# Kernel optimization log

Measured on AMD Instinct MI355X. Metric: run time of the kernel, lower is better.

Reference implementation:

```python
import jax, jax.numpy as jnp
import numpy as np

NEAR_THRESHOLD = 0.3
NUM_HEADING_BIN = 12
NUM_SIZE_CLUSTER = 18
NUM_CLASS = 18
BN_EPS = 1e-5


def setup_inputs() -> dict:
    key = jax.random.key(0)
    ks = jax.random.split(key, 16)
    B, K, C, KG = 256, 256, 128, 64
    OUT = 3 + NUM_HEADING_BIN * 2 + NUM_SIZE_CLUSTER * 4 + NUM_CLASS  # 117
    return {
        "xyz": jax.random.normal(ks[0], (B, K, 3), jnp.float32),
        "features": jax.random.normal(ks[1], (B, C, K), jnp.float32),
        "rn_feature": jax.random.normal(ks[2], (B, C, K), jnp.float32),
        "gt_center": jax.random.normal(ks[3], (B, KG, 3), jnp.float32),
        "objectness_pred": jax.random.randint(ks[4], (B, K), 0, 2, jnp.int64),
        "W1": jax.random.normal(ks[5], (C, 2 * C), jnp.float32) * 0.05,
        "b1": jax.random.normal(ks[6], (C,), jnp.float32) * 0.05,
        "g1": jnp.ones((C,), jnp.float32),
        "be1": jnp.zeros((C,), jnp.float32),
        "W2": jax.random.normal(ks[7], (C, C), jnp.float32) * 0.05,
        "b2": jax.random.normal(ks[8], (C,), jnp.float32) * 0.05,
        "g2": jnp.ones((C,), jnp.float32),
        "be2": jnp.zeros((C,), jnp.float32),
        "W3": jax.random.normal(ks[9], (OUT, C), jnp.float32) * 0.05,
        "b3": jax.random.normal(ks[10], (OUT,), jnp.float32) * 0.05,
        "mean_size": jax.random.uniform(ks[11], (NUM_SIZE_CLUSTER, 3), jnp.float32),
    }


def nn_distance_min(a, b):
    # a: (B,K,3), b: (B,KG,3) -> min squared distance from each a to b
    d = jnp.sum((a[:, :, None, :] - b[:, None, :, :]) ** 2, axis=-1)  # (B,K,KG)
    return jnp.min(d, axis=2)


def get_index(pred):
    # vectorized stream compaction: per row, indices where pred==1 packed first,
    # remaining slots keep arange identity (matches torch get_index semantics).
    B, K = pred.shape
    idx = jnp.arange(K, dtype=jnp.int64)
    key = jnp.where(pred == 1, idx[None, :], idx[None, :] + K)
    srt = jnp.sort(key, axis=1)
    num = jnp.sum(pred, axis=1)  # (B,)
    idx_obj = jnp.where(idx[None, :] < num[:, None], srt, idx[None, :])
    return idx_obj, num


def bn_relu(x, g, b):
    # training-mode BatchNorm1d over (B, C, K): stats over batch+points
    mn = jnp.mean(x, axis=(0, 2), keepdims=True)
    vr = jnp.var(x, axis=(0, 2), keepdims=True)
    xn = (x - mn) * jax.lax.rsqrt(vr + BN_EPS)
    return jax.nn.relu(xn * g[None, :, None] + b[None, :, None])


def reference(xyz, features, rn_feature, gt_center, objectness_pred,
              W1, b1, g1, be1, W2, b2, g2, be2, W3, b3, mean_size):
    B, K, _ = xyz.shape
    # objectness labeling via nn_distance
    dist1 = nn_distance_min(xyz, gt_center)
    euclid = jnp.sqrt(dist1 + 1e-6)
    objectness_label = (euclid < NEAR_THRESHOLD).astype(jnp.int64)
    # stream compaction on predicted objectness
    idx_obj, sum_1 = get_index(objectness_pred)
    # conv1d(k=1) / BN / ReLU head
    feat = jnp.concatenate([features, rn_feature], axis=1)  # (B, 256, K)
    net = bn_relu(jnp.einsum('oc,bck->bok', W1, feat) + b1[None, :, None], g1, be1)
    net = bn_relu(jnp.einsum('oc,bck->bok', W2, net) + b2[None, :, None], g2, be2)
    net = jnp.einsum('oc,bck->bok', W3, net) + b3[None, :, None]  # (B,117,K)
    # decode_scores_pred
    t = jnp.transpose(net, (0, 2, 1))  # (B,K,117)
    nh, ns = NUM_HEADING_BIN, NUM_SIZE_CLUSTER
    center = xyz + t[:, :, 0:3]
    hs = t[:, :, 3:3 + nh]
    hrn = t[:, :, 3 + nh:3 + 2 * nh]
    hr = hrn * (np.pi / nh)
    ss = t[:, :, 3 + 2 * nh:3 + 2 * nh + ns]
    srn = t[:, :, 3 + 2 * nh + ns:3 + 2 * nh + 4 * ns].reshape(B, K, ns, 3)
    sr = srn * mean_size[None, None, :, :]
    sem = t[:, :, 3 + 2 * nh + 4 * ns:]
    out = jnp.concatenate(
        [center, hs, hrn, hr, ss,
         srn.reshape(B, K, ns * 3), sr.reshape(B, K, ns * 3), sem], axis=-1)
    return out, idx_obj, sum_1, objectness_label
```

## Files before the change

kernel.cpp:

```cpp
#include <hip/hip_runtime.h>
#include <hip/hip_bf16.h>
#include <math.h>

#define B_  256
#define K_  256
#define C_  128
#define KG_ 64
#define O3_ 117
#define OD_ 183
#define NPT 65536

typedef unsigned int  u32;
typedef unsigned short u16;
typedef __bf16 bf16_t;
typedef bf16_t bf16x8 __attribute__((ext_vector_type(8)));
typedef float  f32x4  __attribute__((ext_vector_type(4)));

__device__ __forceinline__ float bflo(u32 u){ return __uint_as_float(u << 16); }
__device__ __forceinline__ float bfhi(u32 u){ return __uint_as_float(u & 0xffff0000u); }
__device__ __forceinline__ u16 f2bf(float f){
    __hip_bfloat16 h = __float2bfloat16(f);
    return __builtin_bit_cast(u16, h);
}
__device__ __forceinline__ int swz(int row, int byteInRow){
    return row * 256 + (byteInRow ^ (((row >> 1) & 7) << 4));
}

__global__ __launch_bounds__(256) void prep_kernel(const float* __restrict__ W1,
                                                   const float* __restrict__ W2,
                                                   const float* __restrict__ W3,
                                                   u16* __restrict__ W1bf,
                                                   u16* __restrict__ W2bf,
                                                   u16* __restrict__ W3bf,
                                                   float* __restrict__ accum)
{
    int idx = blockIdx.x * 256 + threadIdx.x;
    if (idx < 512) accum[idx] = 0.0f;
    if (idx < 32768) {
        W1bf[idx] = f2bf(W1[idx]);
    } else if (idx < 49152) {
        int j = idx - 32768;
        W2bf[j] = f2bf(W2[j]);
    } else {
        int j = idx - 49152;
        int row = j >> 7, col = j & 127;
        W3bf[j] = (row < O3_) ? f2bf(W3[row * C_ + col]) : (u16)0;
    }
}

__global__ __launch_bounds__(256) void objness_kernel(const float* __restrict__ xyz,
                                                      const float* __restrict__ gtc,
                                                      float* __restrict__ label)
{
    __shared__ float g[KG_ * 3];
    const int b = blockIdx.x, t = threadIdx.x;
    if (t < KG_ * 3) g[t] = gtc[(size_t)b * KG_ * 3 + t];
    __syncthreads();
    const size_t pidx = (size_t)(b * K_ + t);
    float x = xyz[pidx * 3 + 0];
    float y = xyz[pidx * 3 + 1];
    float z = xyz[pidx * 3 + 2];
    float dmin = 1e30f;
#pragma unroll 8
    for (int j = 0; j < KG_; ++j) {
        float dx = x - g[j * 3 + 0];
        float dy = y - g[j * 3 + 1];
        float dz = z - g[j * 3 + 2];
        float d  = dx * dx + dy * dy + dz * dz;
        dmin = fminf(dmin, d);
    }
    float e = sqrtf(dmin + 1e-6f);
    label[pidx] = (e < 0.3f) ? 1.0f : 0.0f;
}

__global__ __launch_bounds__(256) void getindex_kernel(const int* __restrict__ pred,
                                                       float* __restrict__ idxo,
                                                       float* __restrict__ sum1)
{
    const int b = blockIdx.x, t = threadIdx.x;
    const int p = (pred[b * K_ + t] == 1) ? 1 : 0;
    __shared__ int sd[K_];
    sd[t] = p;
    __syncthreads();
    for (int off = 1; off < K_; off <<= 1) {
        int v = (t >= off) ? sd[t - off] : 0;
        __syncthreads();
        sd[t] += v;
        __syncthreads();
    }
    const int incl = sd[t];
    const int num  = sd[K_ - 1];
    if (t >= num) idxo[b * K_ + t] = (float)t;
    if (p)        idxo[b * K_ + (incl - p)] = (float)t;
    if (t == 0)   sum1[b] = (float)num;
}

__global__ __launch_bounds__(256) void gemm1_kernel(const float* __restrict__ fa,
                                                    const float* __restrict__ fb,
                                                    const u16* __restrict__ Wbf,
                                                    const float* __restrict__ bias,
                                                    u16* __restrict__ outp)
{
    __shared__ __align__(16) char smem[65536];
    const int t   = threadIdx.x;
    const int pt0 = blockIdx.x * 128;
    const int bb  = pt0 >> 8;
    const int k0  = pt0 & 255;
    const int w   = t >> 6, l = t & 63;
    const int lr  = l & 15, lg = l >> 4;

    f32x4 acc[2][8] = {};

    for (int ph = 0; ph < 2; ++ph) {
        if (ph) __syncthreads();
        const float* src = (ph == 0) ? fa : fb;
        {
            const int q  = t & 31;
            const int cb = t >> 5;
#pragma unroll
            for (int j = 0; j < 4; ++j) {
                int cq = cb + j * 8;
                float4 r0 = *(const float4*)(src + ((size_t)(bb*C_ + cq*4 + 0))*K_ + k0 + q*4);
                float4 r1 = *(const float4*)(src + ((size_t)(bb*C_ + cq*4 + 1))*K_ + k0 + q*4);
                float4 r2 = *(const float4*)(src + ((size_t)(bb*C_ + cq*4 + 2))*K_ + k0 + q*4);
                float4 r3 = *(const float4*)(src + ((size_t)(bb*C_ + cq*4 + 3))*K_ + k0 + q*4);
                const float* p0 = (const float*)&r0;
                const float* p1 = (const float*)&r1;
                const float* p2 = (const float*)&r2;
                const float* p3 = (const float*)&r3;
#pragma unroll
                for (int p = 0; p < 4; ++p) {
                    int row = q * 4 + p;
                    uint2 uv;
                    uv.x = (u32)f2bf(p0[p]) | ((u32)f2bf(p1[p]) << 16);
                    uv.y = (u32)f2bf(p2[p]) | ((u32)f2bf(p3[p]) << 16);
                    *(uint2*)(smem + swz(row, cq * 8)) = uv;
                }
            }
        }
        {
            int c8 = (t & 15) * 8;
#pragma unroll
            for (int rr = 0; rr < 8; ++rr) {
                int row = (t >> 4) + rr * 16;
                uint4 v = *(const uint4*)(Wbf + (size_t)row * 256 + ph * 128 + c8);
                *(uint4*)(smem + 32768 + swz(row, c8 * 2)) = v;
            }
        }
        __syncthreads();
#pragma unroll
        for (int ks = 0; ks < 4; ++ks) {
            bf16x8 a[2], bfr[8];
#pragma unroll
            for (int m = 0; m < 2; ++m) {
                int row = w * 32 + m * 16 + lr;
                a[m] = *(const bf16x8*)(smem + swz(row, ks * 64 + lg * 16));
            }
#pragma unroll
            for (int n = 0; n < 8; ++n) {
                int row = n * 16 + lr;
                bfr[n] = *(const bf16x8*)(smem + 32768 + swz(row, ks * 64 + lg * 16));
            }
#pragma unroll
            for (int m = 0; m < 2; ++m)
#pragma unroll
                for (int n = 0; n < 8; ++n)
                    acc[m][n] = __builtin_amdgcn_mfma_f32_16x16x32_bf16(a[m], bfr[n], acc[m][n], 0, 0, 0);
        }
    }
    float bv[8];
#pragma unroll
    for (int n = 0; n < 8; ++n) bv[n] = bias[n * 16 + lr];
#pragma unroll
    for (int m = 0; m < 2; ++m)
#pragma unroll
        for (int n = 0; n < 8; ++n) {
            int o = n * 16 + lr;
#pragma unroll
            for (int r = 0; r < 4; ++r) {
                int row = pt0 + w * 32 + m * 16 + lg * 4 + r;
                outp[(size_t)row * 128 + o] = f2bf(acc[m][n][r] + bv[n]);
            }
        }
}

__global__ __launch_bounds__(256) void stats_kernel(const u16* __restrict__ net,
                                                    float* __restrict__ sumArr,
                                                    float* __restrict__ sqArr)
{
    const int t  = threadIdx.x;
    const int o2 = t & 63;
    const int rg = t >> 6;
    const u32* p = (const u32*)net;
    float sl = 0.f, shi = 0.f, ql = 0.f, qh = 0.f;
    const int base = blockIdx.x * 512 + rg;
    for (int i = 0; i < 128; ++i) {
        u32 v = p[(size_t)(base + i * 4) * 64 + o2];
        float x0 = bflo(v), x1 = bfhi(v);
        sl += x0; shi += x1;
        ql = fmaf(x0, x0, ql); qh = fmaf(x1, x1, qh);
    }
    __shared__ float red[4][64][4];
    red[rg][o2][0] = sl; red[rg][o2][1] = shi;
    red[rg][o2][2] = ql; red[rg][o2][3] = qh;
    __syncthreads();
    if (t < 64) {
        float a0 = 0, a1 = 0, a2 = 0, a3 = 0;
#pragma unroll
        for (int r = 0; r < 4; ++r) {
            a0 += red[r][t][0]; a1 += red[r][t][1];
            a2 += red[r][t][2]; a3 += red[r][t][3];
        }
        atomicAdd(&sumArr[2 * t],     a0);
        atomicAdd(&sumArr[2 * t + 1], a1);
        atomicAdd(&sqArr[2 * t],      a2);
        atomicAdd(&sqArr[2 * t + 1],  a3);
    }
}

__global__ __launch_bounds__(128) void finalize_kernel(const float* __restrict__ sum,
                                                       const float* __restrict__ sq,
                                                       const float* __restrict__ g,
                                                       const float* __restrict__ be,
                                                       float* __restrict__ sc,
                                                       float* __restrict__ sh)
{
    int c = threadIdx.x;
    const float inv = 1.0f / 65536.0f;
    float mean = sum[c] * inv;
    float var  = sq[c] * inv - mean * mean;
    float s = g[c] * rsqrtf(var + 1e-5f);
    sc[c] = s;
    sh[c] = be[c] - mean * s;
}

__global__ __launch_bounds__(256) void gemm2_kernel(const u16* __restrict__ inp,
                                                    const float* __restrict__ sc,
                                                    const float* __restrict__ sh,
                                                    const u16* __restrict__ Wbf,
                                                    const float* __restrict__ bias,
                                                    u16* __restrict__ outp)
{
    __shared__ __align__(16) char smem[65536];
    const int t   = threadIdx.x;
    const int pt0 = blockIdx.x * 128;
    const int w   = t >> 6, l = t & 63;
    const int lr  = l & 15, lg = l >> 4;

    {
        int c8 = (t & 15) * 8;
        float s0[8], t0[8];
#pragma unroll
        for (int j = 0; j < 8; ++j) { s0[j] = sc[c8 + j]; t0[j] = sh[c8 + j]; }
#pragma unroll
        for (int rr = 0; rr < 8; ++rr) {
            int row = (t >> 4) + rr * 16;
            uint4 v = *(const uint4*)(inp + (size_t)(pt0 + row) * 128 + c8);
            u32 vv[4] = {v.x, v.y, v.z, v.w};
            u32 ov[4];
#pragma unroll
            for (int k = 0; k < 4; ++k) {
                float x0 = fmaxf(0.f, fmaf(bflo(vv[k]), s0[2 * k],     t0[2 * k]));
                float x1 = fmaxf(0.f, fmaf(bfhi(vv[k]), s0[2 * k + 1], t0[2 * k + 1]));
                ov[k] = (u32)f2bf(x0) | ((u32)f2bf(x1) << 16);
            }
            uint4 q; q.x = ov[0]; q.y = ov[1]; q.z = ov[2]; q.w = ov[3];
            *(uint4*)(smem + swz(row, c8 * 2)) = q;
        }
#pragma unroll
        for (int rr = 0; rr < 8; ++rr) {
            int row = (t >> 4) + rr * 16;
            uint4 v = *(const uint4*)(Wbf + (size_t)row * 128 + c8);
            *(uint4*)(smem + 32768 + swz(row, c8 * 2)) = v;
        }
    }
    __syncthreads();

    f32x4 acc[2][8] = {};
#pragma unroll
    for (int ks = 0; ks < 4; ++ks) {
        bf16x8 a[2], bfr[8];
#pragma unroll
        for (int m = 0; m < 2; ++m) {
            int row = w * 32 + m * 16 + lr;
            a[m] = *(const bf16x8*)(smem + swz(row, ks * 64 + lg * 16));
        }
#pragma unroll
        for (int n = 0; n < 8; ++n) {
            int row = n * 16 + lr;
            bfr[n] = *(const bf16x8*)(smem + 32768 + swz(row, ks * 64 + lg * 16));
        }
#pragma unroll
        for (int m = 0; m < 2; ++m)
#pragma unroll
            for (int n = 0; n < 8; ++n)
                acc[m][n] = __builtin_amdgcn_mfma_f32_16x16x32_bf16(a[m], bfr[n], acc[m][n], 0, 0, 0);
    }

    float bv[8];
#pragma unroll
    for (int n = 0; n < 8; ++n) bv[n] = bias[n * 16 + lr];
#pragma unroll
    for (int m = 0; m < 2; ++m)
#pragma unroll
        for (int n = 0; n < 8; ++n) {
            int o = n * 16 + lr;
#pragma unroll
            for (int r = 0; r < 4; ++r) {
                int row = pt0 + w * 32 + m * 16 + lg * 4 + r;
                outp[(size_t)row * 128 + o] = f2bf(acc[m][n][r] + bv[n]);
            }
        }
}

__global__ __launch_bounds__(256) void gemm3_kernel(const u16* __restrict__ inp,
                                                    const float* __restrict__ sc,
                                                    const float* __restrict__ sh,
                                                    const u16* __restrict__ Wbf,
                                                    const float* __restrict__ bias,
                                                    const float* __restrict__ xyz,
                                                    const float* __restrict__ msize,
                                                    float* __restrict__ out)
{
    __shared__ __align__(16) char smem[65536];
    const int t   = threadIdx.x;
    const int pt0 = blockIdx.x * 128;
    const int w   = t >> 6, l = t & 63;
    const int lr  = l & 15, lg = l >> 4;

    {
        int c8 = (t & 15) * 8;
        float s0[8], t0[8];
#pragma unroll
        for (int j = 0; j < 8; ++j) { s0[j] = sc[c8 + j]; t0[j] = sh[c8 + j]; }
#pragma unroll
        for (int rr = 0; rr < 8; ++rr) {
            int row = (t >> 4) + rr * 16;
            uint4 v = *(const uint4*)(inp + (size_t)(pt0 + row) * 128 + c8);
            u32 vv[4] = {v.x, v.y, v.z, v.w};
            u32 ov[4];
#pragma unroll
            for (int k = 0; k < 4; ++k) {
                float x0 = fmaxf(0.f, fmaf(bflo(vv[k]), s0[2 * k],     t0[2 * k]));
                float x1 = fmaxf(0.f, fmaf(bfhi(vv[k]), s0[2 * k + 1], t0[2 * k + 1]));
                ov[k] = (u32)f2bf(x0) | ((u32)f2bf(x1) << 16);
            }
            uint4 q; q.x = ov[0]; q.y = ov[1]; q.z = ov[2]; q.w = ov[3];
            *(uint4*)(smem + swz(row, c8 * 2)) = q;
        }
#pragma unroll
        for (int rr = 0; rr < 8; ++rr) {
            int row = (t >> 4) + rr * 16;
            uint4 v = *(const uint4*)(Wbf + (size_t)row * 128 + c8);
            *(uint4*)(smem + 32768 + swz(row, c8 * 2)) = v;
        }
    }
    __syncthreads();

    f32x4 acc[2][8] = {};
#pragma unroll
    for (int ks = 0; ks < 4; ++ks) {
        bf16x8 a[2], bfr[8];
#pragma unroll
        for (int m = 0; m < 2; ++m) {
            int row = w * 32 + m * 16 + lr;
            a[m] = *(const bf16x8*)(smem + swz(row, ks * 64 + lg * 16));
        }
#pragma unroll
        for (int n = 0; n < 8; ++n) {
            int row = n * 16 + lr;
            bfr[n] = *(const bf16x8*)(smem + 32768 + swz(row, ks * 64 + lg * 16));
        }
#pragma unroll
        for (int m = 0; m < 2; ++m)
#pragma unroll
            for (int n = 0; n < 8; ++n)
                acc[m][n] = __builtin_amdgcn_mfma_f32_16x16x32_bf16(a[m], bfr[n], acc[m][n], 0, 0, 0);
    }

    const float PI12 = 0.26179938779914946f;
    for (int s = 0; s < 2; ++s) {
        __syncthreads();
        if ((w >> 1) == s) {
            float* Of = (float*)smem + (w & 1) * (32 * 184);
#pragma unroll
            for (int n = 0; n < 8; ++n) {
                int o = n * 16 + lr;
                if (o < O3_) {
                    float bvn = bias[o];
                    float msv = (o >= 45 && o < 99) ? msize[o - 45] : 0.f;
#pragma unroll
                    for (int m = 0; m < 2; ++m)
#pragma unroll
                        for (int r = 0; r < 4; ++r) {
                            int pl = m * 16 + lg * 4 + r;
                            float v = acc[m][n][r] + bvn;
                            float* row = Of + pl * 184;
                            if (o < 3) {
                                int gp = pt0 + w * 32 + pl;
                                row[o] = v + xyz[(size_t)gp * 3 + o];
                            } else if (o < 15) {
                                row[o] = v;
                            } else if (o < 27) {
                                row[o] = v; row[o + 12] = v * PI12;
                            } else if (o < 45) {
                                row[o + 12] = v;
                            } else if (o < 99) {
                                row[o + 12] = v; row[o + 66] = v * msv;
                            } else {
                                row[o + 66] = v;
                            }
                        }
                }
            }
        }
        __syncthreads();
        float* Ob = out + (size_t)(pt0 + s * 64) * OD_;
        const float* Sf = (const float*)smem;
        for (int i = t; i < 64 * OD_; i += 256) {
            int pl  = (int)(((u32)i * 91680u) >> 24);
            int col = i - pl * 183;
            Ob[i] = Sf[(pl >> 5) * (32 * 184) + (pl & 31) * 184 + col];
        }
    }
}

extern "C" void kernel_launch(void* const* d_in, const int* in_sizes, int n_in,
                              void* d_out, int out_size, void* d_ws, size_t ws_size,
                              hipStream_t stream)
{
    const float* xyz      = (const float*)d_in[0];
    const float* features = (const float*)d_in[1];
    const float* rn       = (const float*)d_in[2];
    const float* gtc      = (const float*)d_in[3];
    const int*   pred     = (const int*)d_in[4];
    const float* W1  = (const float*)d_in[5];
    const float* b1  = (const float*)d_in[6];
    const float* g1  = (const float*)d_in[7];
    const float* be1 = (const float*)d_in[8];
    const float* W2  = (const float*)d_in[9];
    const float* b2  = (const float*)d_in[10];
    const float* g2  = (const float*)d_in[11];
    const float* be2 = (const float*)d_in[12];
    const float* W3  = (const float*)d_in[13];
    const float* b3  = (const float*)d_in[14];
    const float* ms  = (const float*)d_in[15];

    float* out = (float*)d_out;
    const size_t OFF_IDX = (size_t)B_ * K_ * OD_;
    const size_t OFF_SUM = OFF_IDX + (size_t)B_ * K_;
    const size_t OFF_LAB = OFF_SUM + B_;

    char* ws = (char*)d_ws;
    u16*  net1 = (u16*)ws;
    u16*  net2 = (u16*)(ws + 16777216);
    u16*  W1bf = (u16*)(ws + 33554432);
    u16*  W2bf = (u16*)(ws + 33619968);
    u16*  W3bf = (u16*)(ws + 33652736);
    float* accb = (float*)(ws + 33685504);
    float* sum1 = accb;          float* sq1 = accb + 128;
    float* sum2 = accb + 256;    float* sq2 = accb + 384;
    float* sc1  = accb + 512;    float* sh1 = accb + 640;
    float* sc2  = accb + 768;    float* sh2 = accb + 896;

    prep_kernel<<<256, 256, 0, stream>>>(W1, W2, W3, W1bf, W2bf, W3bf, accb);
    objness_kernel<<<B_, 256, 0, stream>>>(xyz, gtc, out + OFF_LAB);
    getindex_kernel<<<B_, 256, 0, stream>>>(pred, out + OFF_IDX, out + OFF_SUM);

    gemm1_kernel<<<512, 256, 0, stream>>>(features, rn, W1bf, b1, net1);
    stats_kernel<<<128, 256, 0, stream>>>(net1, sum1, sq1);
    finalize_kernel<<<1, 128, 0, stream>>>(sum1, sq1, g1, be1, sc1, sh1);

    gemm2_kernel<<<512, 256, 0, stream>>>(net1, sc1, sh1, W2bf, b2, net2);
    stats_kernel<<<128, 256, 0, stream>>>(net2, sum2, sq2);
    finalize_kernel<<<1, 128, 0, stream>>>(sum2, sq2, g2, be2, sc2, sh2);

    gemm3_kernel<<<512, 256, 0, stream>>>(net2, sc2, sh2, W3bf, b3, xyz, ms, out);
}
```

Measured before the change: 209.0 us.

## Fuse BN statistics into GEMM epilogues and merge small prep kernels

Each GEMM epilogue now stages its output tile in shared memory, stores it coalesced in a channel-major tile layout, and writes per-block partial sums and sums of squares. This removes the separate stats kernels and their atomics. The finalize kernel reduces the 512 partials per channel in parallel. The prep, objectness and get-index kernels are merged into one launch, and the later GEMMs read the new tile layout through a reworked BN staging routine. The cost is extra shared-memory traffic and syncs in the epilogue, plus partial buffers in the workspace.

```diff
diff --git a/kernel.cpp b/kernel.cpp
--- a/kernel.cpp
+++ b/kernel.cpp
@@ -8,7 +8,6 @@
 #define KG_ 64
 #define O3_ 117
 #define OD_ 183
-#define NPT 65536
 
 typedef unsigned int  u32;
 typedef unsigned short u16;
@@ -26,84 +25,206 @@
     return row * 256 + (byteInRow ^ (((row >> 1) & 7) << 4));
 }
 
-__global__ __launch_bounds__(256) void prep_kernel(const float* __restrict__ W1,
+__global__ __launch_bounds__(256) void misc_kernel(const float* __restrict__ xyz,
+                                                   const float* __restrict__ gtc,
+                                                   const int*   __restrict__ pred,
+                                                   const float* __restrict__ W1,
                                                    const float* __restrict__ W2,
                                                    const float* __restrict__ W3,
                                                    u16* __restrict__ W1bf,
                                                    u16* __restrict__ W2bf,
                                                    u16* __restrict__ W3bf,
-                                                   float* __restrict__ accum)
-{
-    int idx = blockIdx.x * 256 + threadIdx.x;
-    if (idx < 512) accum[idx] = 0.0f;
-    if (idx < 32768) {
-        W1bf[idx] = f2bf(W1[idx]);
-    } else if (idx < 49152) {
-        int j = idx - 32768;
-        W2bf[j] = f2bf(W2[j]);
+                                                   float* __restrict__ label,
+                                                   float* __restrict__ idxo,
+                                                   float* __restrict__ sum1)
+{
+    const int blk = blockIdx.x, t = threadIdx.x;
+    if (blk < 256) {
+        __shared__ float g[KG_ * 3];
+        const int b = blk;
+        if (t < KG_ * 3) g[t] = gtc[(size_t)b * KG_ * 3 + t];
+        __syncthreads();
+        const size_t pidx = (size_t)(b * K_ + t);
+        float x = xyz[pidx * 3 + 0];
+        float y = xyz[pidx * 3 + 1];
+        float z = xyz[pidx * 3 + 2];
+        float dmin = 1e30f;
+#pragma unroll 8
+        for (int j = 0; j < KG_; ++j) {
+            float dx = x - g[j * 3 + 0];
+            float dy = y - g[j * 3 + 1];
+            float dz = z - g[j * 3 + 2];
+            float d  = dx * dx + dy * dy + dz * dz;
+            dmin = fminf(dmin, d);
+        }
+        float e = sqrtf(dmin + 1e-6f);
+        label[pidx] = (e < 0.3f) ? 1.0f : 0.0f;
+    } else if (blk < 512) {
+        const int b = blk - 256;
+        const int p = (pred[b * K_ + t] == 1) ? 1 : 0;
+        __shared__ int sd[K_];
+        sd[t] = p;
+        __syncthreads();
+        for (int off = 1; off < K_; off <<= 1) {
+            int v = (t >= off) ? sd[t - off] : 0;
+            __syncthreads();
+            sd[t] += v;
+            __syncthreads();
+        }
+        const int incl = sd[t];
+        const int num  = sd[K_ - 1];
+        if (t >= num) idxo[b * K_ + t] = (float)t;
+        if (p)        idxo[b * K_ + (incl - p)] = (float)t;
+        if (t == 0)   sum1[b] = (float)num;
     } else {
-        int j = idx - 49152;
-        int row = j >> 7, col = j & 127;
-        W3bf[j] = (row < O3_) ? f2bf(W3[row * C_ + col]) : (u16)0;
-    }
-}
-
-__global__ __launch_bounds__(256) void objness_kernel(const float* __restrict__ xyz,
-                                                      const float* __restrict__ gtc,
-                                                      float* __restrict__ label)
-{
-    __shared__ float g[KG_ * 3];
-    const int b = blockIdx.x, t = threadIdx.x;
-    if (t < KG_ * 3) g[t] = gtc[(size_t)b * KG_ * 3 + t];
+        int idx = (blk - 512) * 256 + t;
+        if (idx < 32768) {
+            W1bf[idx] = f2bf(W1[idx]);
+        } else if (idx < 49152) {
+            int j = idx - 32768;
+            W2bf[j] = f2bf(W2[j]);
+        } else {
+            int j = idx - 49152;
+            int row = j >> 7, col = j & 127;
+            W3bf[j] = (row < O3_) ? f2bf(W3[row * C_ + col]) : (u16)0;
+        }
+    }
+}
+
+__device__ __forceinline__ void epilogue_store(char* smem, const f32x4 acc[2][8],
+                                               const float* __restrict__ bias,
+                                               u16* __restrict__ outp, float* __restrict__ part,
+                                               int pb, int t, int w, int lr, int lg)
+{
+    float* SP = (float*)(smem + 40960);
+    float* SQ = (float*)(smem + 49152);
+#pragma unroll
+    for (int n = 0; n < 8; ++n) {
+        int o = n * 16 + lr;
+        float bvn = bias[o];
+        float s = 0.f, q = 0.f;
+#pragma unroll
+        for (int m = 0; m < 2; ++m) {
+            float v0 = acc[m][n][0] + bvn;
+            float v1 = acc[m][n][1] + bvn;
+            float v2 = acc[m][n][2] + bvn;
+            float v3 = acc[m][n][3] + bvn;
+            s += (v0 + v1) + (v2 + v3);
+            q = fmaf(v0, v0, q); q = fmaf(v1, v1, q);
+            q = fmaf(v2, v2, q); q = fmaf(v3, v3, q);
+            uint2 pk;
+            pk.x = (u32)f2bf(v0) | ((u32)f2bf(v1) << 16);
+            pk.y = (u32)f2bf(v2) | ((u32)f2bf(v3) << 16);
+            *(uint2*)(smem + o * 264 + (w * 32 + m * 16 + lg * 4) * 2) = pk;
+        }
+        SP[(w * 4 + lg) * 128 + o] = s;
+        SQ[(w * 4 + lg) * 128 + o] = q;
+    }
     __syncthreads();
-    const size_t pidx = (size_t)(b * K_ + t);
-    float x = xyz[pidx * 3 + 0];
-    float y = xyz[pidx * 3 + 1];
-    float z = xyz[pidx * 3 + 2];
-    float dmin = 1e30f;
-#pragma unroll 8
-    for (int j = 0; j < KG_; ++j) {
-        float dx = x - g[j * 3 + 0];
-        float dy = y - g[j * 3 + 1];
-        float dz = z - g[j * 3 + 2];
-        float d  = dx * dx + dy * dy + dz * dz;
-        dmin = fminf(dmin, d);
-    }
-    float e = sqrtf(dmin + 1e-6f);
-    label[pidx] = (e < 0.3f) ? 1.0f : 0.0f;
-}
-
-__global__ __launch_bounds__(256) void getindex_kernel(const int* __restrict__ pred,
-                                                       float* __restrict__ idxo,
-                                                       float* __restrict__ sum1)
-{
-    const int b = blockIdx.x, t = threadIdx.x;
-    const int p = (pred[b * K_ + t] == 1) ? 1 : 0;
-    __shared__ int sd[K_];
-    sd[t] = p;
-    __syncthreads();
-    for (int off = 1; off < K_; off <<= 1) {
-        int v = (t >= off) ? sd[t - off] : 0;
-        __syncthreads();
-        sd[t] += v;
-        __syncthreads();
-    }
-    const int incl = sd[t];
-    const int num  = sd[K_ - 1];
-    if (t >= num) idxo[b * K_ + t] = (float)t;
-    if (p)        idxo[b * K_ + (incl - p)] = (float)t;
-    if (t == 0)   sum1[b] = (float)num;
+    u16* dst = outp + (size_t)pb * 16384;
+#pragma unroll
+    for (int j = 0; j < 8; ++j) {
+        int i = t + j * 256;
+        int c = i >> 4, col = i & 15;
+        uint4 v = *(const uint4*)(smem + c * 264 + col * 16);
+        *(uint4*)(dst + c * 128 + col * 8) = v;
+    }
+    if (t < 128) {
+        float s = 0.f, q = 0.f;
+#pragma unroll
+        for (int i = 0; i < 16; ++i) { s += SP[i * 128 + t]; q += SQ[i * 128 + t]; }
+        part[pb * 256 + t] = s;
+        part[pb * 256 + 128 + t] = q;
+    }
+}
+
+__device__ __forceinline__ void stage_bn(char* smem, const u16* __restrict__ net,
+                                         const float* __restrict__ sc,
+                                         const float* __restrict__ sh, int pb, int t)
+{
+    const u16* tile = net + (size_t)pb * 16384;
+    const int q = t & 15, cb = t >> 4;
+#pragma unroll
+    for (int j = 0; j < 2; ++j) {
+        int c0 = j * 64 + cb * 4;
+        u32 R[4][4];
+#pragma unroll
+        for (int i2 = 0; i2 < 4; ++i2) {
+            uint4 v = *(const uint4*)(tile + (c0 + i2) * 128 + q * 8);
+            R[i2][0] = v.x; R[i2][1] = v.y; R[i2][2] = v.z; R[i2][3] = v.w;
+        }
+        float ss[4], tt[4];
+#pragma unroll
+        for (int i2 = 0; i2 < 4; ++i2) { ss[i2] = sc[c0 + i2]; tt[i2] = sh[c0 + i2]; }
+#pragma unroll
+        for (int p = 0; p < 8; ++p) {
+            int wi = p >> 1;
+            float f0, f1, f2, f3;
+            if (p & 1) {
+                f0 = bfhi(R[0][wi]); f1 = bfhi(R[1][wi]);
+                f2 = bfhi(R[2][wi]); f3 = bfhi(R[3][wi]);
+            } else {
+                f0 = bflo(R[0][wi]); f1 = bflo(R[1][wi]);
+                f2 = bflo(R[2][wi]); f3 = bflo(R[3][wi]);
+            }
+            f0 = fmaxf(0.f, fmaf(f0, ss[0], tt[0]));
+            f1 = fmaxf(0.f, fmaf(f1, ss[1], tt[1]));
+            f2 = fmaxf(0.f, fmaf(f2, ss[2], tt[2]));
+            f3 = fmaxf(0.f, fmaf(f3, ss[3], tt[3]));
+            uint2 pk;
+            pk.x = (u32)f2bf(f0) | ((u32)f2bf(f1) << 16);
+            pk.y = (u32)f2bf(f2) | ((u32)f2bf(f3) << 16);
+            int row = q * 8 + p;
+            *(uint2*)(smem + swz(row, c0 * 2)) = pk;
+        }
+    }
+}
+
+__device__ __forceinline__ void stage_w128(char* smem, const u16* __restrict__ Wbf, int t)
+{
+    int c8 = (t & 15) * 8;
+#pragma unroll
+    for (int rr = 0; rr < 8; ++rr) {
+        int row = (t >> 4) + rr * 16;
+        uint4 v = *(const uint4*)(Wbf + (size_t)row * 128 + c8);
+        *(uint4*)(smem + 32768 + swz(row, c8 * 2)) = v;
+    }
+}
+
+__device__ __forceinline__ void compute_tile(char* smem, f32x4 acc[2][8], int w, int lr, int lg)
+{
+#pragma unroll
+    for (int ks = 0; ks < 4; ++ks) {
+        bf16x8 a[2], bfr[8];
+#pragma unroll
+        for (int m = 0; m < 2; ++m) {
+            int row = w * 32 + m * 16 + lr;
+            a[m] = *(const bf16x8*)(smem + swz(row, ks * 64 + lg * 16));
+        }
+#pragma unroll
+        for (int n = 0; n < 8; ++n) {
+            int row = n * 16 + lr;
+            bfr[n] = *(const bf16x8*)(smem + 32768 + swz(row, ks * 64 + lg * 16));
+        }
+#pragma unroll
+        for (int m = 0; m < 2; ++m)
+#pragma unroll
+            for (int n = 0; n < 8; ++n)
+                acc[m][n] = __builtin_amdgcn_mfma_f32_16x16x32_bf16(a[m], bfr[n], acc[m][n], 0, 0, 0);
+    }
 }
 
 __global__ __launch_bounds__(256) void gemm1_kernel(const float* __restrict__ fa,
                                                     const float* __restrict__ fb,
                                                     const u16* __restrict__ Wbf,
                                                     const float* __restrict__ bias,
-                                                    u16* __restrict__ outp)
+                                                    u16* __restrict__ outp,
+                                                    float* __restrict__ part)
 {
     __shared__ __align__(16) char smem[65536];
     const int t   = threadIdx.x;
-    const int pt0 = blockIdx.x * 128;
+    const int pb  = blockIdx.x;
+    const int pt0 = pb * 128;
     const int bb  = pt0 >> 8;
     const int k0  = pt0 & 255;
     const int w   = t >> 6, l = t & 63;
@@ -148,172 +269,66 @@
             }
         }
         __syncthreads();
-#pragma unroll
-        for (int ks = 0; ks < 4; ++ks) {
-            bf16x8 a[2], bfr[8];
-#pragma unroll
-            for (int m = 0; m < 2; ++m) {
-                int row = w * 32 + m * 16 + lr;
-                a[m] = *(const bf16x8*)(smem + swz(row, ks * 64 + lg * 16));
-            }
-#pragma unroll
-            for (int n = 0; n < 8; ++n) {
-                int row = n * 16 + lr;
-                bfr[n] = *(const bf16x8*)(smem + 32768 + swz(row, ks * 64 + lg * 16));
-            }
-#pragma unroll
-            for (int m = 0; m < 2; ++m)
-#pragma unroll
-                for (int n = 0; n < 8; ++n)
-                    acc[m][n] = __builtin_amdgcn_mfma_f32_16x16x32_bf16(a[m], bfr[n], acc[m][n], 0, 0, 0);
-        }
-    }
-    float bv[8];
-#pragma unroll
-    for (int n = 0; n < 8; ++n) bv[n] = bias[n * 16 + lr];
-#pragma unroll
-    for (int m = 0; m < 2; ++m)
-#pragma unroll
-        for (int n = 0; n < 8; ++n) {
-            int o = n * 16 + lr;
-#pragma unroll
-            for (int r = 0; r < 4; ++r) {
-                int row = pt0 + w * 32 + m * 16 + lg * 4 + r;
-                outp[(size_t)row * 128 + o] = f2bf(acc[m][n][r] + bv[n]);
-            }
-        }
-}
-
-__global__ __launch_bounds__(256) void stats_kernel(const u16* __restrict__ net,
-                                                    float* __restrict__ sumArr,
-                                                    float* __restrict__ sqArr)
-{
-    const int t  = threadIdx.x;
-    const int o2 = t & 63;
-    const int rg = t >> 6;
-    const u32* p = (const u32*)net;
-    float sl = 0.f, shi = 0.f, ql = 0.f, qh = 0.f;
-    const int base = blockIdx.x * 512 + rg;
-    for (int i = 0; i < 128; ++i) {
-        u32 v = p[(size_t)(base + i * 4) * 64 + o2];
-        float x0 = bflo(v), x1 = bfhi(v);
-        sl += x0; shi += x1;
-        ql = fmaf(x0, x0, ql); qh = fmaf(x1, x1, qh);
-    }
-    __shared__ float red[4][64][4];
-    red[rg][o2][0] = sl; red[rg][o2][1] = shi;
-    red[rg][o2][2] = ql; red[rg][o2][3] = qh;
+        compute_tile(smem, acc, w, lr, lg);
+    }
     __syncthreads();
-    if (t < 64) {
-        float a0 = 0, a1 = 0, a2 = 0, a3 = 0;
-#pragma unroll
-        for (int r = 0; r < 4; ++r) {
-            a0 += red[r][t][0]; a1 += red[r][t][1];
-            a2 += red[r][t][2]; a3 += red[r][t][3];
-        }
-        atomicAdd(&sumArr[2 * t],     a0);
-        atomicAdd(&sumArr[2 * t + 1], a1);
-        atomicAdd(&sqArr[2 * t],      a2);
-        atomicAdd(&sqArr[2 * t + 1],  a3);
-    }
-}
-
-__global__ __launch_bounds__(128) void finalize_kernel(const float* __restrict__ sum,
-                                                       const float* __restrict__ sq,
-                                                       const float* __restrict__ g,
-                                                       const float* __restrict__ be,
-                                                       float* __restrict__ sc,
-                                                       float* __restrict__ sh)
-{
-    int c = threadIdx.x;
-    const float inv = 1.0f / 65536.0f;
-    float mean = sum[c] * inv;
-    float var  = sq[c] * inv - mean * mean;
-    float s = g[c] * rsqrtf(var + 1e-5f);
-    sc[c] = s;
-    sh[c] = be[c] - mean * s;
-}
-
-__global__ __launch_bounds__(256) void gemm2_kernel(const u16* __restrict__ inp,
+    epilogue_store(smem, acc, bias, outp, part, pb, t, w, lr, lg);
+}
+
+__global__ __launch_bounds__(64) void finalize_kernel(const float* __restrict__ part,
+                                                      const float* __restrict__ g,
+                                                      const float* __restrict__ be,
+                                                      float* __restrict__ sc,
+                                                      float* __restrict__ sh)
+{
+    const int c = blockIdx.x, l = threadIdx.x;
+    float s = 0.f, q = 0.f;
+#pragma unroll
+    for (int i = 0; i < 8; ++i) {
+        int pb = l + i * 64;
+        s += part[pb * 256 + c];
+        q += part[pb * 256 + 128 + c];
+    }
+#pragma unroll
+    for (int off = 32; off > 0; off >>= 1) {
+        s += __shfl_down(s, off);
+        q += __shfl_down(q, off);
+    }
+    if (l == 0) {
+        const float inv = 1.0f / 65536.0f;
+        float mean = s * inv;
+        float var  = q * inv - mean * mean;
+        float scv  = g[c] * rsqrtf(var + 1e-5f);
+        sc[c] = scv;
+        sh[c] = be[c] - mean * scv;
+    }
+}
+
+__global__ __launch_bounds__(256) void gemm2_kernel(const u16* __restrict__ net,
                                                     const float* __restrict__ sc,
                                                     const float* __restrict__ sh,
                                                     const u16* __restrict__ Wbf,
                                                     const float* __restrict__ bias,
-                                                    u16* __restrict__ outp)
+                                                    u16* __restrict__ outp,
+                                                    float* __restrict__ part)
 {
     __shared__ __align__(16) char smem[65536];
-    const int t   = threadIdx.x;
-    const int pt0 = blockIdx.x * 128;
-    const int w   = t >> 6, l = t & 63;
-    const int lr  = l & 15, lg = l >> 4;
-
-    {
-        int c8 = (t & 15) * 8;
-        float s0[8], t0[8];
-#pragma unroll
-        for (int j = 0; j < 8; ++j) { s0[j] = sc[c8 + j]; t0[j] = sh[c8 + j]; }
-#pragma unroll
-        for (int rr = 0; rr < 8; ++rr) {
-            int row = (t >> 4) + rr * 16;
-            uint4 v = *(const uint4*)(inp + (size_t)(pt0 + row) * 128 + c8);
-            u32 vv[4] = {v.x, v.y, v.z, v.w};
-            u32 ov[4];
-#pragma unroll
-            for (int k = 0; k < 4; ++k) {
-                float x0 = fmaxf(0.f, fmaf(bflo(vv[k]), s0[2 * k],     t0[2 * k]));
-                float x1 = fmaxf(0.f, fmaf(bfhi(vv[k]), s0[2 * k + 1], t0[2 * k + 1]));
-                ov[k] = (u32)f2bf(x0) | ((u32)f2bf(x1) << 16);
-            }
-            uint4 q; q.x = ov[0]; q.y = ov[1]; q.z = ov[2]; q.w = ov[3];
-            *(uint4*)(smem + swz(row, c8 * 2)) = q;
-        }
-#pragma unroll
-        for (int rr = 0; rr < 8; ++rr) {
-            int row = (t >> 4) + rr * 16;
-            uint4 v = *(const uint4*)(Wbf + (size_t)row * 128 + c8);
-            *(uint4*)(smem + 32768 + swz(row, c8 * 2)) = v;
-        }
-    }
+    const int t  = threadIdx.x;
+    const int pb = blockIdx.x;
+    const int w  = t >> 6, l = t & 63;
+    const int lr = l & 15, lg = l >> 4;
+
+    stage_bn(smem, net, sc, sh, pb, t);
+    stage_w128(smem, Wbf, t);
     __syncthreads();
 
     f32x4 acc[2][8] = {};
-#pragma unroll
-    for (int ks = 0; ks < 4; ++ks) {
-        bf16x8 a[2], bfr[8];
-#pragma unroll
-        for (int m = 0; m < 2; ++m) {
-            int row = w * 32 + m * 16 + lr;
-            a[m] = *(const bf16x8*)(smem + swz(row, ks * 64 + lg * 16));
-        }
-#pragma unroll
-        for (int n = 0; n < 8; ++n) {
-            int row = n * 16 + lr;
-            bfr[n] = *(const bf16x8*)(smem + 32768 + swz(row, ks * 64 + lg * 16));
-        }
-#pragma unroll
-        for (int m = 0; m < 2; ++m)
-#pragma unroll
-            for (int n = 0; n < 8; ++n)
-                acc[m][n] = __builtin_amdgcn_mfma_f32_16x16x32_bf16(a[m], bfr[n], acc[m][n], 0, 0, 0);
-    }
-
-    float bv[8];
-#pragma unroll
-    for (int n = 0; n < 8; ++n) bv[n] = bias[n * 16 + lr];
-#pragma unroll
-    for (int m = 0; m < 2; ++m)
-#pragma unroll
-        for (int n = 0; n < 8; ++n) {
-            int o = n * 16 + lr;
-#pragma unroll
-            for (int r = 0; r < 4; ++r) {
-                int row = pt0 + w * 32 + m * 16 + lg * 4 + r;
-                outp[(size_t)row * 128 + o] = f2bf(acc[m][n][r] + bv[n]);
-            }
-        }
-}
-
-__global__ __launch_bounds__(256) void gemm3_kernel(const u16* __restrict__ inp,
+    compute_tile(smem, acc, w, lr, lg);
+    __syncthreads();
+    epilogue_store(smem, acc, bias, outp, part, pb, t, w, lr, lg);
+}
+
+__global__ __launch_bounds__(256) void gemm3_kernel(const u16* __restrict__ net,
                                                     const float* __restrict__ sc,
                                                     const float* __restrict__ sh,
                                                     const u16* __restrict__ Wbf,
@@ -324,59 +339,17 @@
 {
     __shared__ __align__(16) char smem[65536];
     const int t   = threadIdx.x;
-    const int pt0 = blockIdx.x * 128;
+    const int pb  = blockIdx.x;
+    const int pt0 = pb * 128;
     const int w   = t >> 6, l = t & 63;
     const int lr  = l & 15, lg = l >> 4;
 
-    {
-        int c8 = (t & 15) * 8;
-        float s0[8], t0[8];
-#pragma unroll
-        for (int j = 0; j < 8; ++j) { s0[j] = sc[c8 + j]; t0[j] = sh[c8 + j]; }
-#pragma unroll
-        for (int rr = 0; rr < 8; ++rr) {
-            int row = (t >> 4) + rr * 16;
-            uint4 v = *(const uint4*)(inp + (size_t)(pt0 + row) * 128 + c8);
-            u32 vv[4] = {v.x, v.y, v.z, v.w};
-            u32 ov[4];
-#pragma unroll
-            for (int k = 0; k < 4; ++k) {
-                float x0 = fmaxf(0.f, fmaf(bflo(vv[k]), s0[2 * k],     t0[2 * k]));
-                float x1 = fmaxf(0.f, fmaf(bfhi(vv[k]), s0[2 * k + 1], t0[2 * k + 1]));
-                ov[k] = (u32)f2bf(x0) | ((u32)f2bf(x1) << 16);
-            }
-            uint4 q; q.x = ov[0]; q.y = ov[1]; q.z = ov[2]; q.w = ov[3];
-            *(uint4*)(smem + swz(row, c8 * 2)) = q;
-        }
-#pragma unroll
-        for (int rr = 0; rr < 8; ++rr) {
-            int row = (t >> 4) + rr * 16;
-            uint4 v = *(const uint4*)(Wbf + (size_t)row * 128 + c8);
-            *(uint4*)(smem + 32768 + swz(row, c8 * 2)) = v;
-        }
-    }
+    stage_bn(smem, net, sc, sh, pb, t);
+    stage_w128(smem, Wbf, t);
     __syncthreads();
 
     f32x4 acc[2][8] = {};
-#pragma unroll
-    for (int ks = 0; ks < 4; ++ks) {
-        bf16x8 a[2], bfr[8];
-#pragma unroll
-        for (int m = 0; m < 2; ++m) {
-            int row = w * 32 + m * 16 + lr;
-            a[m] = *(const bf16x8*)(smem + swz(row, ks * 64 + lg * 16));
-        }
-#pragma unroll
-        for (int n = 0; n < 8; ++n) {
-            int row = n * 16 + lr;
-            bfr[n] = *(const bf16x8*)(smem + 32768 + swz(row, ks * 64 + lg * 16));
-        }
-#pragma unroll
-        for (int m = 0; m < 2; ++m)
-#pragma unroll
-            for (int n = 0; n < 8; ++n)
-                acc[m][n] = __builtin_amdgcn_mfma_f32_16x16x32_bf16(a[m], bfr[n], acc[m][n], 0, 0, 0);
-    }
+    compute_tile(smem, acc, w, lr, lg);
 
     const float PI12 = 0.26179938779914946f;
     for (int s = 0; s < 2; ++s) {
@@ -457,23 +430,21 @@
     u16*  W1bf = (u16*)(ws + 33554432);
     u16*  W2bf = (u16*)(ws + 33619968);
     u16*  W3bf = (u16*)(ws + 33652736);
-    float* accb = (float*)(ws + 33685504);
-    float* sum1 = accb;          float* sq1 = accb + 128;
-    float* sum2 = accb + 256;    float* sq2 = accb + 384;
-    float* sc1  = accb + 512;    float* sh1 = accb + 640;
-    float* sc2  = accb + 768;    float* sh2 = accb + 896;
-
-    prep_kernel<<<256, 256, 0, stream>>>(W1, W2, W3, W1bf, W2bf, W3bf, accb);
-    objness_kernel<<<B_, 256, 0, stream>>>(xyz, gtc, out + OFF_LAB);
-    getindex_kernel<<<B_, 256, 0, stream>>>(pred, out + OFF_IDX, out + OFF_SUM);
-
-    gemm1_kernel<<<512, 256, 0, stream>>>(features, rn, W1bf, b1, net1);
-    stats_kernel<<<128, 256, 0, stream>>>(net1, sum1, sq1);
-    finalize_kernel<<<1, 128, 0, stream>>>(sum1, sq1, g1, be1, sc1, sh1);
-
-    gemm2_kernel<<<512, 256, 0, stream>>>(net1, sc1, sh1, W2bf, b2, net2);
-    stats_kernel<<<128, 256, 0, stream>>>(net2, sum2, sq2);
-    finalize_kernel<<<1, 128, 0, stream>>>(sum2, sq2, g2, be2, sc2, sh2);
+    float* part1 = (float*)(ws + 33685504);
+    float* part2 = (float*)(ws + 34209792);
+    float* coef  = (float*)(ws + 34734080);
+    float* sc1 = coef;        float* sh1 = coef + 128;
+    float* sc2 = coef + 256;  float* sh2 = coef + 384;
+
+    misc_kernel<<<768, 256, 0, stream>>>(xyz, gtc, pred, W1, W2, W3,
+                                         W1bf, W2bf, W3bf,
+                                         out + OFF_LAB, out + OFF_IDX, out + OFF_SUM);
+
+    gemm1_kernel<<<512, 256, 0, stream>>>(features, rn, W1bf, b1, net1, part1);
+    finalize_kernel<<<128, 64, 0, stream>>>(part1, g1, be1, sc1, sh1);
+
+    gemm2_kernel<<<512, 256, 0, stream>>>(net1, sc1, sh1, W2bf, b2, net2, part2);
+    finalize_kernel<<<128, 64, 0, stream>>>(part2, g2, be2, sc2, sh2);
 
     gemm3_kernel<<<512, 256, 0, stream>>>(net2, sc2, sh2, W3bf, b3, xyz, ms, out);
 }
```

New measurement: 183.9 us. 1.14x faster.
